# Optimization experiments

Measured on AMD Instinct MI355X. Metric: run time of the kernel, lower is better.

## Reference

```python
import jax, jax.numpy as jnp
import numpy as np

K = 2          # number of pool_types ('max','avg') -> mixture components
HID = 32       # selector hidden width (Conv2d(channels,32,1))
KH = KW = 3    # conv_pool kernel_size=3, padding=1


def setup_inputs() -> dict:
    key = jax.random.key(0)
    ks = jax.random.split(key, 6)
    B, C, H, W = 16, 128, 192, 192
    x = jax.random.normal(ks[0], (B, C, H, W), jnp.float32)
    # selector: 1x1 convs == linear layers on globally-pooled features
    w1 = jax.random.normal(ks[1], (HID, C), jnp.float32) * (1.0 / np.sqrt(C))
    b1 = jnp.zeros((HID,), jnp.float32)
    w2 = jax.random.normal(ks[2], (K, HID), jnp.float32) * (1.0 / np.sqrt(HID))
    b2 = jnp.zeros((K,), jnp.float32)
    # bank of K depthwise kernels: [K, out_channels=C, C//groups=1, kh, kw]
    weight_bank = jax.random.normal(ks[3], (K, C, 1, KH, KW), jnp.float32) * (1.0 / 3.0)
    bias = jax.random.normal(ks[4], (C,), jnp.float32) * 0.01
    return {"x": x, "w1": w1, "b1": b1, "w2": w2, "b2": b2,
            "weight_bank": weight_bank, "bias": bias}


def reference(x, w1, b1, w2, b2, weight_bank, bias):
    B, C, H, W = x.shape
    # --- selector head: AdaptiveAvgPool2d(1) -> 1x1 conv -> ReLU -> 1x1 conv -> softmax ---
    pooled = x.mean(axis=(2, 3))                              # [B, C]
    h = jax.nn.relu(pooled @ w1.T + b1)                       # [B, HID]
    attn = jax.nn.softmax(h @ w2.T + b2, axis=1)              # [B, K]
    # --- per-sample dynamic kernel combination ---
    # [B,K] x [K,C,1,kh,kw] -> [B,C,1,kh,kw]
    cw = jnp.einsum('bk,koihw->boihw', attn, weight_bank)
    # --- batched depthwise conv via groups = B*C (x viewed as [1, B*C, H, W]) ---
    lhs = x.reshape(1, B * C, H, W)
    rhs = cw.reshape(B * C, 1, KH, KW)
    out = jax.lax.conv_general_dilated(
        lhs, rhs,
        window_strides=(1, 1),
        padding=((1, 1), (1, 1)),
        feature_group_count=B * C,
        dimension_numbers=('NCHW', 'OIHW', 'NCHW'))
    out = out.reshape(B, C, H, W) + bias[None, :, None, None]
    return out
```

## Files before the change

### kernel.cpp

```cpp
#include <hip/hip_runtime.h>
#include <hip/hip_bf16.h>

#define B 16
#define C 128
#define H 192
#define W 192
#define HID 32
#define K 2
#define PLANE (H*W)
#define NPLANES (B*C)

#define TBLK 384
#define TROWS 32
#define SROWS 34
#define LDST 196
#define SEGS (H / TROWS)

#define CHUNK_SAMP 4
#define CHUNK_PLANES (CHUNK_SAMP * C)
#define NCHUNKS (B / CHUNK_SAMP)

typedef float floatx4 __attribute__((ext_vector_type(4)));

__global__ __launch_bounds__(TBLK) void fused_kernel(const float* __restrict__ x,
                                                     const float* __restrict__ w1,
                                                     const float* __restrict__ b1,
                                                     const float* __restrict__ w2,
                                                     const float* __restrict__ b2,
                                                     const float* __restrict__ wb,
                                                     const float* __restrict__ bias,
                                                     float* __restrict__ pooled,
                                                     float* __restrict__ out,
                                                     int convBase, int poolBase,
                                                     int doConv, int doPool) {
    const int tid = threadIdx.x;

    bool isPool;
    int poolPlane = 0, convPlane = 0, seg = 0;
    if (doPool && doConv) {
        const int g = blockIdx.x / 7, r = blockIdx.x % 7;
        isPool = (r == 6);
        poolPlane = poolBase + g;
        convPlane = convBase + g;
        seg = r;
    } else if (doPool) {
        isPool = true;
        poolPlane = poolBase + blockIdx.x;
    } else {
        isPool = false;
        convPlane = convBase + blockIdx.x / SEGS;
        seg = blockIdx.x % SEGS;
    }

    if (isPool) {
        __shared__ float red[TBLK / 64];
        const float4* px4 = (const float4*)(x + (size_t)poolPlane * PLANE);
        float s = 0.f;
        #pragma unroll
        for (int it = 0; it < PLANE / 4 / TBLK; ++it) {
            float4 v = px4[tid + it * TBLK];
            s += v.x + v.y + v.z + v.w;
        }
        for (int off = 32; off; off >>= 1) s += __shfl_down(s, off, 64);
        const int lane = tid & 63, wid = tid >> 6;
        if (lane == 0) red[wid] = s;
        __syncthreads();
        if (tid == 0) {
            float t = 0.f;
            #pragma unroll
            for (int wv = 0; wv < TBLK / 64; ++wv) t += red[wv];
            pooled[poolPlane] = t * (1.0f / (float)PLANE);
        }
        return;
    }

    __shared__ float lds[SROWS * LDST];
    __shared__ float sh[HID];
    __shared__ float sAtt[K];
    __shared__ float sw[9];

    const int plane = convPlane;
    const int c     = plane & (C - 1);
    const int smp   = plane >> 7;
    const int y0    = seg * TROWS;

    const float4* px4 = (const float4*)(x + (size_t)plane * PLANE);
    float4* lds4 = (float4*)lds;
    #pragma unroll
    for (int k = 0; k < 5; ++k) {
        const int idx = tid + k * TBLK;
        if (idx < SROWS * 48) {
            const int row  = idx / 48;
            const int col4 = idx % 48;
            const int gRow = y0 - 1 + row;
            float4 v = make_float4(0.f, 0.f, 0.f, 0.f);
            if (gRow >= 0 && gRow < H) v = px4[gRow * 48 + col4];
            lds4[row * 49 + col4] = v;
        }
    }

    if (tid < HID) {
        float s = b1[tid];
        const float* pb = pooled + smp * C;
        const float* wj = w1 + tid * C;
        #pragma unroll 8
        for (int cc = 0; cc < C; ++cc) s += pb[cc] * wj[cc];
        sh[tid] = fmaxf(s, 0.f);
    }
    __syncthreads();
    if (tid < K) {
        float s = b2[tid];
        const float* wk = w2 + tid * HID;
        #pragma unroll
        for (int j = 0; j < HID; ++j) s += sh[j] * wk[j];
        sAtt[tid] = s;
    }
    __syncthreads();
    if (tid == 0) {
        const float a0 = sAtt[0], a1 = sAtt[1];
        const float m = fmaxf(a0, a1);
        const float e0 = __expf(a0 - m), e1 = __expf(a1 - m);
        const float inv = 1.f / (e0 + e1);
        sAtt[0] = e0 * inv;
        sAtt[1] = e1 * inv;
    }
    __syncthreads();
    if (tid < 9) {
        sw[tid] = sAtt[0] * wb[c * 9 + tid] + sAtt[1] * wb[C * 9 + c * 9 + tid];
    }
    __syncthreads();

    const float w00 = sw[0], w01 = sw[1], w02 = sw[2];
    const float w10 = sw[3], w11 = sw[4], w12 = sw[5];
    const float w20 = sw[6], w21 = sw[7], w22 = sw[8];
    const float bv = bias[c];

    const int xq   = tid % 48;
    const int band = tid / 48;
    const int x0   = xq * 4;

    float acc[4][4];
    #pragma unroll
    for (int j = 0; j < 4; ++j) {
        acc[j][0] = bv; acc[j][1] = bv; acc[j][2] = bv; acc[j][3] = bv;
    }

    #pragma unroll
    for (int i = 0; i < 6; ++i) {
        const int sr = band * 4 + i;
        const float* lr = lds + sr * LDST;
        const floatx4 cur = *(const floatx4*)(lr + x0);
        const float v0 = (xq > 0)  ? lr[x0 - 1] : 0.f;
        const float v5 = (xq < 47) ? lr[x0 + 4] : 0.f;
        const float v1 = cur.x, v2 = cur.y, v3 = cur.z, v4 = cur.w;

        if (i < 4) {
            acc[i][0] = fmaf(w00, v0, fmaf(w01, v1, fmaf(w02, v2, acc[i][0])));
            acc[i][1] = fmaf(w00, v1, fmaf(w01, v2, fmaf(w02, v3, acc[i][1])));
            acc[i][2] = fmaf(w00, v2, fmaf(w01, v3, fmaf(w02, v4, acc[i][2])));
            acc[i][3] = fmaf(w00, v3, fmaf(w01, v4, fmaf(w02, v5, acc[i][3])));
        }
        if (i >= 1 && i <= 4) {
            acc[i-1][0] = fmaf(w10, v0, fmaf(w11, v1, fmaf(w12, v2, acc[i-1][0])));
            acc[i-1][1] = fmaf(w10, v1, fmaf(w11, v2, fmaf(w12, v3, acc[i-1][1])));
            acc[i-1][2] = fmaf(w10, v2, fmaf(w11, v3, fmaf(w12, v4, acc[i-1][2])));
            acc[i-1][3] = fmaf(w10, v3, fmaf(w11, v4, fmaf(w12, v5, acc[i-1][3])));
        }
        if (i >= 2) {
            acc[i-2][0] = fmaf(w20, v0, fmaf(w21, v1, fmaf(w22, v2, acc[i-2][0])));
            acc[i-2][1] = fmaf(w20, v1, fmaf(w21, v2, fmaf(w22, v3, acc[i-2][1])));
            acc[i-2][2] = fmaf(w20, v2, fmaf(w21, v3, fmaf(w22, v4, acc[i-2][2])));
            acc[i-2][3] = fmaf(w20, v3, fmaf(w21, v4, fmaf(w22, v5, acc[i-2][3])));
        }
    }

    float* po = out + (size_t)plane * PLANE + (y0 + band * 4) * W + x0;
    #pragma unroll
    for (int j = 0; j < 4; ++j) {
        floatx4 o = { acc[j][0], acc[j][1], acc[j][2], acc[j][3] };
        __builtin_nontemporal_store(o, (floatx4*)(po + j * W));
    }
}

extern "C" void kernel_launch(void* const* d_in, const int* in_sizes, int n_in,
                              void* d_out, int out_size, void* d_ws, size_t ws_size,
                              hipStream_t stream) {
    const float* x    = (const float*)d_in[0];
    const float* w1   = (const float*)d_in[1];
    const float* b1   = (const float*)d_in[2];
    const float* w2   = (const float*)d_in[3];
    const float* b2   = (const float*)d_in[4];
    const float* wb   = (const float*)d_in[5];
    const float* bias = (const float*)d_in[6];
    float* out = (float*)d_out;

    float* pooled = (float*)d_ws;

    fused_kernel<<<CHUNK_PLANES, TBLK, 0, stream>>>(
        x, w1, b1, w2, b2, wb, bias, pooled, out,
        0, 0, 0, 1);

    for (int c = 0; c < NCHUNKS - 1; ++c) {
        fused_kernel<<<CHUNK_PLANES * 7, TBLK, 0, stream>>>(
            x, w1, b1, w2, b2, wb, bias, pooled, out,
            c * CHUNK_PLANES, (c + 1) * CHUNK_PLANES, 1, 1);
    }

    fused_kernel<<<CHUNK_PLANES * SEGS, TBLK, 0, stream>>>(
        x, w1, b1, w2, b2, wb, bias, pooled, out,
        (NCHUNKS - 1) * CHUNK_PLANES, 0, 1, 0);
}
```

Baseline: 190.6 us.

## Replace chunked multi-launch pipeline with persistent work-queue kernel and atomic dependencies

Swaps the sequence of chunked launches for a single persistent kernel. Blocks pull tasks from an atomic counter: plane pooling first, then a per-sample selector, then conv tiles. The selector runs once per sample and publishes the combined kernel weights, and conv tiles spin on a per-sample flag, so launch gaps and repeated selector math per block go away. In exchange it adds a memset launch, atomic and spin-wait overhead, and relies on the ordered task queue to avoid deadlock.

```diff
diff --git a/kernel.cpp b/kernel.cpp
--- a/kernel.cpp
+++ b/kernel.cpp
@@ -16,169 +16,187 @@
 #define LDST 196
 #define SEGS (H / TROWS)
 
-#define CHUNK_SAMP 4
-#define CHUNK_PLANES (CHUNK_SAMP * C)
-#define NCHUNKS (B / CHUNK_SAMP)
+#define NPOOL   NPLANES
+#define NSEL    B
+#define NCONV   (NPLANES * SEGS)
+#define NTASKS  (NPOOL + NSEL + NCONV)
+#define GRID    1280
+
+#define AGENT __HIP_MEMORY_SCOPE_AGENT
 
 typedef float floatx4 __attribute__((ext_vector_type(4)));
 
-__global__ __launch_bounds__(TBLK) void fused_kernel(const float* __restrict__ x,
-                                                     const float* __restrict__ w1,
-                                                     const float* __restrict__ b1,
-                                                     const float* __restrict__ w2,
-                                                     const float* __restrict__ b2,
-                                                     const float* __restrict__ wb,
-                                                     const float* __restrict__ bias,
-                                                     float* __restrict__ pooled,
-                                                     float* __restrict__ out,
-                                                     int convBase, int poolBase,
-                                                     int doConv, int doPool) {
+__global__ __launch_bounds__(TBLK) void persist_kernel(
+        const float* __restrict__ x,
+        const float* __restrict__ w1, const float* __restrict__ b1,
+        const float* __restrict__ w2, const float* __restrict__ b2,
+        const float* __restrict__ wb, const float* __restrict__ bias,
+        unsigned int* __restrict__ ctr,
+        unsigned int* __restrict__ done,
+        unsigned int* __restrict__ selDone,
+        float* __restrict__ pooled,
+        float* __restrict__ cwA,
+        float* __restrict__ out) {
     const int tid = threadIdx.x;
 
-    bool isPool;
-    int poolPlane = 0, convPlane = 0, seg = 0;
-    if (doPool && doConv) {
-        const int g = blockIdx.x / 7, r = blockIdx.x % 7;
-        isPool = (r == 6);
-        poolPlane = poolBase + g;
-        convPlane = convBase + g;
-        seg = r;
-    } else if (doPool) {
-        isPool = true;
-        poolPlane = poolBase + blockIdx.x;
-    } else {
-        isPool = false;
-        convPlane = convBase + blockIdx.x / SEGS;
-        seg = blockIdx.x % SEGS;
-    }
-
-    if (isPool) {
-        __shared__ float red[TBLK / 64];
-        const float4* px4 = (const float4*)(x + (size_t)poolPlane * PLANE);
-        float s = 0.f;
-        #pragma unroll
-        for (int it = 0; it < PLANE / 4 / TBLK; ++it) {
-            float4 v = px4[tid + it * TBLK];
-            s += v.x + v.y + v.z + v.w;
+    __shared__ float lds[SROWS * LDST];
+    __shared__ float sw[12];
+    __shared__ int   sTask;
+
+    for (;;) {
+        if (tid == 0) sTask = (int)atomicAdd(ctr, 1u);
+        __syncthreads();
+        const int t = sTask;
+        if (t >= NTASKS) return;
+
+        if (t < NPOOL) {
+            const int p = t;
+            const float4* px4 = (const float4*)(x + (size_t)p * PLANE);
+            float s = 0.f;
+            #pragma unroll
+            for (int it = 0; it < PLANE / 4 / TBLK; ++it) {
+                float4 v = px4[tid + it * TBLK];
+                s += v.x + v.y + v.z + v.w;
+            }
+            for (int off = 32; off; off >>= 1) s += __shfl_down(s, off, 64);
+            const int lane = tid & 63, wid = tid >> 6;
+            if (lane == 0) lds[wid] = s;
+            __syncthreads();
+            if (tid == 0) {
+                float m = (lds[0] + lds[1] + lds[2] + lds[3] + lds[4] + lds[5])
+                          * (1.0f / (float)PLANE);
+                __hip_atomic_store(&pooled[p], m, __ATOMIC_RELAXED, AGENT);
+                __hip_atomic_fetch_add(&done[p >> 7], 1u, __ATOMIC_RELEASE, AGENT);
+            }
+        } else if (t < NPOOL + NSEL) {
+            const int s = t - NPOOL;
+            if (tid == 0) {
+                while (__hip_atomic_load(&done[s], __ATOMIC_ACQUIRE, AGENT) < 128u)
+                    __builtin_amdgcn_s_sleep(32);
+            }
+            __syncthreads();
+            float* sh   = lds;
+            float* sAtt = lds + 64;
+            if (tid < HID) {
+                float acc = b1[tid];
+                const float* wj = w1 + tid * C;
+                #pragma unroll 8
+                for (int cc = 0; cc < C; ++cc) {
+                    float pv = __hip_atomic_load(&pooled[s * C + cc], __ATOMIC_RELAXED, AGENT);
+                    acc = fmaf(pv, wj[cc], acc);
+                }
+                sh[tid] = fmaxf(acc, 0.f);
+            }
+            __syncthreads();
+            if (tid < K) {
+                float acc = b2[tid];
+                const float* wk = w2 + tid * HID;
+                #pragma unroll
+                for (int j = 0; j < HID; ++j) acc = fmaf(sh[j], wk[j], acc);
+                sAtt[tid] = acc;
+            }
+            __syncthreads();
+            if (tid == 0) {
+                const float a0 = sAtt[0], a1 = sAtt[1];
+                const float m = fmaxf(a0, a1);
+                const float e0 = __expf(a0 - m), e1 = __expf(a1 - m);
+                const float inv = 1.f / (e0 + e1);
+                sAtt[0] = e0 * inv;
+                sAtt[1] = e1 * inv;
+            }
+            __syncthreads();
+            const float a0 = sAtt[0], a1 = sAtt[1];
+            for (int i = tid; i < C * 9; i += TBLK) {
+                float v = a0 * wb[i] + a1 * wb[C * 9 + i];
+                __hip_atomic_store(&cwA[s * C * 9 + i], v, __ATOMIC_RELAXED, AGENT);
+            }
+            __syncthreads();
+            if (tid == 0)
+                __hip_atomic_store(&selDone[s], 1u, __ATOMIC_RELEASE, AGENT);
+        } else {
+            const int tt    = t - NPOOL - NSEL;
+            const int plane = tt / SEGS;
+            const int seg   = tt % SEGS;
+            const int c     = plane & (C - 1);
+            const int s     = plane >> 7;
+            const int y0    = seg * TROWS;
+
+            const float4* px4 = (const float4*)(x + (size_t)plane * PLANE);
+            float4* lds4 = (float4*)lds;
+            #pragma unroll
+            for (int k = 0; k < 5; ++k) {
+                const int idx = tid + k * TBLK;
+                if (idx < SROWS * 48) {
+                    const int row  = idx / 48;
+                    const int col4 = idx % 48;
+                    const int gRow = y0 - 1 + row;
+                    float4 v = make_float4(0.f, 0.f, 0.f, 0.f);
+                    if (gRow >= 0 && gRow < H) v = px4[gRow * 48 + col4];
+                    lds4[row * 49 + col4] = v;
+                }
+            }
+            if (tid == 0) {
+                while (!__hip_atomic_load(&selDone[s], __ATOMIC_ACQUIRE, AGENT))
+                    __builtin_amdgcn_s_sleep(16);
+            }
+            __syncthreads();
+            if (tid < 9)
+                sw[tid] = __hip_atomic_load(&cwA[(size_t)s * C * 9 + c * 9 + tid],
+                                            __ATOMIC_RELAXED, AGENT);
+            __syncthreads();
+
+            const float w00 = sw[0], w01 = sw[1], w02 = sw[2];
+            const float w10 = sw[3], w11 = sw[4], w12 = sw[5];
+            const float w20 = sw[6], w21 = sw[7], w22 = sw[8];
+            const float bv = bias[c];
+
+            const int xq   = tid % 48;
+            const int band = tid / 48;
+            const int x0   = xq * 4;
+
+            float acc[4][4];
+            #pragma unroll
+            for (int j = 0; j < 4; ++j) {
+                acc[j][0] = bv; acc[j][1] = bv; acc[j][2] = bv; acc[j][3] = bv;
+            }
+
+            #pragma unroll
+            for (int i = 0; i < 6; ++i) {
+                const int sr = band * 4 + i;
+                const float* lr = lds + sr * LDST;
+                const floatx4 cur = *(const floatx4*)(lr + x0);
+                const float v0 = (xq > 0)  ? lr[x0 - 1] : 0.f;
+                const float v5 = (xq < 47) ? lr[x0 + 4] : 0.f;
+                const float v1 = cur.x, v2 = cur.y, v3 = cur.z, v4 = cur.w;
+
+                if (i < 4) {
+                    acc[i][0] = fmaf(w00, v0, fmaf(w01, v1, fmaf(w02, v2, acc[i][0])));
+                    acc[i][1] = fmaf(w00, v1, fmaf(w01, v2, fmaf(w02, v3, acc[i][1])));
+                    acc[i][2] = fmaf(w00, v2, fmaf(w01, v3, fmaf(w02, v4, acc[i][2])));
+                    acc[i][3] = fmaf(w00, v3, fmaf(w01, v4, fmaf(w02, v5, acc[i][3])));
+                }
+                if (i >= 1 && i <= 4) {
+                    acc[i-1][0] = fmaf(w10, v0, fmaf(w11, v1, fmaf(w12, v2, acc[i-1][0])));
+                    acc[i-1][1] = fmaf(w10, v1, fmaf(w11, v2, fmaf(w12, v3, acc[i-1][1])));
+                    acc[i-1][2] = fmaf(w10, v2, fmaf(w11, v3, fmaf(w12, v4, acc[i-1][2])));
+                    acc[i-1][3] = fmaf(w10, v3, fmaf(w11, v4, fmaf(w12, v5, acc[i-1][3])));
+                }
+                if (i >= 2) {
+                    acc[i-2][0] = fmaf(w20, v0, fmaf(w21, v1, fmaf(w22, v2, acc[i-2][0])));
+                    acc[i-2][1] = fmaf(w20, v1, fmaf(w21, v2, fmaf(w22, v3, acc[i-2][1])));
+                    acc[i-2][2] = fmaf(w20, v2, fmaf(w21, v3, fmaf(w22, v4, acc[i-2][2])));
+                    acc[i-2][3] = fmaf(w20, v3, fmaf(w21, v4, fmaf(w22, v5, acc[i-2][3])));
+                }
+            }
+
+            float* po = out + (size_t)plane * PLANE + (y0 + band * 4) * W + x0;
+            #pragma unroll
+            for (int j = 0; j < 4; ++j) {
+                floatx4 o = { acc[j][0], acc[j][1], acc[j][2], acc[j][3] };
+                __builtin_nontemporal_store(o, (floatx4*)(po + j * W));
+            }
         }
-        for (int off = 32; off; off >>= 1) s += __shfl_down(s, off, 64);
-        const int lane = tid & 63, wid = tid >> 6;
-        if (lane == 0) red[wid] = s;
         __syncthreads();
-        if (tid == 0) {
-            float t = 0.f;
-            #pragma unroll
-            for (int wv = 0; wv < TBLK / 64; ++wv) t += red[wv];
-            pooled[poolPlane] = t * (1.0f / (float)PLANE);
-        }
-        return;
-    }
-
-    __shared__ float lds[SROWS * LDST];
-    __shared__ float sh[HID];
-    __shared__ float sAtt[K];
-    __shared__ float sw[9];
-
-    const int plane = convPlane;
-    const int c     = plane & (C - 1);
-    const int smp   = plane >> 7;
-    const int y0    = seg * TROWS;
-
-    const float4* px4 = (const float4*)(x + (size_t)plane * PLANE);
-    float4* lds4 = (float4*)lds;
-    #pragma unroll
-    for (int k = 0; k < 5; ++k) {
-        const int idx = tid + k * TBLK;
-        if (idx < SROWS * 48) {
-            const int row  = idx / 48;
-            const int col4 = idx % 48;
-            const int gRow = y0 - 1 + row;
-            float4 v = make_float4(0.f, 0.f, 0.f, 0.f);
-            if (gRow >= 0 && gRow < H) v = px4[gRow * 48 + col4];
-            lds4[row * 49 + col4] = v;
-        }
-    }
-
-    if (tid < HID) {
-        float s = b1[tid];
-        const float* pb = pooled + smp * C;
-        const float* wj = w1 + tid * C;
-        #pragma unroll 8
-        for (int cc = 0; cc < C; ++cc) s += pb[cc] * wj[cc];
-        sh[tid] = fmaxf(s, 0.f);
-    }
-    __syncthreads();
-    if (tid < K) {
-        float s = b2[tid];
-        const float* wk = w2 + tid * HID;
-        #pragma unroll
-        for (int j = 0; j < HID; ++j) s += sh[j] * wk[j];
-        sAtt[tid] = s;
-    }
-    __syncthreads();
-    if (tid == 0) {
-        const float a0 = sAtt[0], a1 = sAtt[1];
-        const float m = fmaxf(a0, a1);
-        const float e0 = __expf(a0 - m), e1 = __expf(a1 - m);
-        const float inv = 1.f / (e0 + e1);
-        sAtt[0] = e0 * inv;
-        sAtt[1] = e1 * inv;
-    }
-    __syncthreads();
-    if (tid < 9) {
-        sw[tid] = sAtt[0] * wb[c * 9 + tid] + sAtt[1] * wb[C * 9 + c * 9 + tid];
-    }
-    __syncthreads();
-
-    const float w00 = sw[0], w01 = sw[1], w02 = sw[2];
-    const float w10 = sw[3], w11 = sw[4], w12 = sw[5];
-    const float w20 = sw[6], w21 = sw[7], w22 = sw[8];
-    const float bv = bias[c];
-
-    const int xq   = tid % 48;
-    const int band = tid / 48;
-    const int x0   = xq * 4;
-
-    float acc[4][4];
-    #pragma unroll
-    for (int j = 0; j < 4; ++j) {
-        acc[j][0] = bv; acc[j][1] = bv; acc[j][2] = bv; acc[j][3] = bv;
-    }
-
-    #pragma unroll
-    for (int i = 0; i < 6; ++i) {
-        const int sr = band * 4 + i;
-        const float* lr = lds + sr * LDST;
-        const floatx4 cur = *(const floatx4*)(lr + x0);
-        const float v0 = (xq > 0)  ? lr[x0 - 1] : 0.f;
-        const float v5 = (xq < 47) ? lr[x0 + 4] : 0.f;
-        const float v1 = cur.x, v2 = cur.y, v3 = cur.z, v4 = cur.w;
-
-        if (i < 4) {
-            acc[i][0] = fmaf(w00, v0, fmaf(w01, v1, fmaf(w02, v2, acc[i][0])));
-            acc[i][1] = fmaf(w00, v1, fmaf(w01, v2, fmaf(w02, v3, acc[i][1])));
-            acc[i][2] = fmaf(w00, v2, fmaf(w01, v3, fmaf(w02, v4, acc[i][2])));
-            acc[i][3] = fmaf(w00, v3, fmaf(w01, v4, fmaf(w02, v5, acc[i][3])));
-        }
-        if (i >= 1 && i <= 4) {
-            acc[i-1][0] = fmaf(w10, v0, fmaf(w11, v1, fmaf(w12, v2, acc[i-1][0])));
-            acc[i-1][1] = fmaf(w10, v1, fmaf(w11, v2, fmaf(w12, v3, acc[i-1][1])));
-            acc[i-1][2] = fmaf(w10, v2, fmaf(w11, v3, fmaf(w12, v4, acc[i-1][2])));
-            acc[i-1][3] = fmaf(w10, v3, fmaf(w11, v4, fmaf(w12, v5, acc[i-1][3])));
-        }
-        if (i >= 2) {
-            acc[i-2][0] = fmaf(w20, v0, fmaf(w21, v1, fmaf(w22, v2, acc[i-2][0])));
-            acc[i-2][1] = fmaf(w20, v1, fmaf(w21, v2, fmaf(w22, v3, acc[i-2][1])));
-            acc[i-2][2] = fmaf(w20, v2, fmaf(w21, v3, fmaf(w22, v4, acc[i-2][2])));
-            acc[i-2][3] = fmaf(w20, v3, fmaf(w21, v4, fmaf(w22, v5, acc[i-2][3])));
-        }
-    }
-
-    float* po = out + (size_t)plane * PLANE + (y0 + band * 4) * W + x0;
-    #pragma unroll
-    for (int j = 0; j < 4; ++j) {
-        floatx4 o = { acc[j][0], acc[j][1], acc[j][2], acc[j][3] };
-        __builtin_nontemporal_store(o, (floatx4*)(po + j * W));
     }
 }
 
@@ -194,19 +212,15 @@
     const float* bias = (const float*)d_in[6];
     float* out = (float*)d_out;
 
-    float* pooled = (float*)d_ws;
-
-    fused_kernel<<<CHUNK_PLANES, TBLK, 0, stream>>>(
-        x, w1, b1, w2, b2, wb, bias, pooled, out,
-        0, 0, 0, 1);
-
-    for (int c = 0; c < NCHUNKS - 1; ++c) {
-        fused_kernel<<<CHUNK_PLANES * 7, TBLK, 0, stream>>>(
-            x, w1, b1, w2, b2, wb, bias, pooled, out,
-            c * CHUNK_PLANES, (c + 1) * CHUNK_PLANES, 1, 1);
-    }
-
-    fused_kernel<<<CHUNK_PLANES * SEGS, TBLK, 0, stream>>>(
-        x, w1, b1, w2, b2, wb, bias, pooled, out,
-        (NCHUNKS - 1) * CHUNK_PLANES, 0, 1, 0);
+    unsigned int* ctr     = (unsigned int*)d_ws;
+    unsigned int* done    = ctr + 32;
+    unsigned int* selDone = ctr + 64;
+    float* pooled = (float*)(ctr + 256);
+    float* cwA    = pooled + NPLANES;
+
+    const size_t zbytes = (256 + NPLANES + NPLANES * 9) * sizeof(float);
+    hipMemsetAsync(d_ws, 0, zbytes, stream);
+
+    persist_kernel<<<GRID, TBLK, 0, stream>>>(x, w1, b1, w2, b2, wb, bias,
+                                              ctr, done, selDone, pooled, cwA, out);
 }
```

Result: slower. 312.2 us (+63.8%).
